# Kernel optimization log

Hardware: AMD Instinct MI355X
Metric: run time of the kernel (lower is better)

Reference implementation:

```python
import jax, jax.numpy as jnp
import numpy as np

NEG = -9.0e15
BN_EPS = 1e-5


def _build_graph():
    N = 22
    A = np.eye(N, dtype=np.float32)
    for i in range(N - 1):
        A[i, i + 1] = 1.0
        A[i + 1, i] = 1.0
    distal = [3, 7, 11, 15, 16, 20, 21]
    jl = [0, 1, 2, 3, 17, 18, 19, 20, 21]
    jr = [4, 5, 6, 7, 12, 13, 14, 15, 16]
    adj_sym = np.zeros((N, N), dtype=np.float32)
    for i in range(N):
        adj_sym[i, i] = 1.0
        if i in jl:
            adj_sym[i, jr[jl.index(i)]] = 1.0
        if i in jr:
            adj_sym[i, jl[jr.index(i)]] = 1.0
    A1 = A.copy()
    for i in distal:
        A1[i] = 0.0
    A2 = np.linalg.matrix_power(A, 2)
    A3 = np.linalg.matrix_power(A, 3)
    for i in range(N):
        if i not in distal:
            A2[i] = 0.0
            A3[i] = 0.0
    adj_con = A1 + A2 + A3
    return adj_sym, adj_con


def setup_inputs() -> dict:
    key = jax.random.key(0)
    B, T, N, C, O = 64, 50, 22, 64, 64
    adj_sym, adj_con = _build_graph()
    rs, cs = np.nonzero(adj_sym > 0)  # row-major, matches torch nonzero order
    rc, cc = np.nonzero(adj_con > 0)
    ks = jax.random.split(key, 11)
    f32 = jnp.float32
    return {
        "x": jax.random.normal(ks[0], (B, T, N, C), f32),
        "W_sym": 0.1 * jax.random.normal(ks[1], (2, C, O), f32),
        "e_sym": 1.0 + 0.1 * jax.random.normal(ks[2], (O, len(rs)), f32),
        "W_con": 0.1 * jax.random.normal(ks[3], (2, C, O), f32),
        "e_con": 1.0 + 0.1 * jax.random.normal(ks[4], (O, len(rc)), f32),
        "W_dis": 0.1 * jax.random.normal(ks[5], (C, O), f32),
        "att": 0.1 * jax.random.normal(ks[6], (N, N), f32),
        "b_dis": 0.1 * jax.random.normal(ks[7], (O,), f32),
        "cat_w": 0.05 * jax.random.normal(ks[8], (O, 3 * O), f32),
        "gammas": 1.0 + 0.1 * jax.random.normal(ks[9], (4, O), f32),
        "betas": 0.1 * jax.random.normal(ks[10], (4, O), f32),
        "rows_sym": jnp.asarray(rs, jnp.int32),
        "cols_sym": jnp.asarray(cs, jnp.int32),
        "rows_con": jnp.asarray(rc, jnp.int32),
        "cols_con": jnp.asarray(cc, jnp.int32),
    }


def _semch(x, W, e, rows, cols):
    # x: [B,T,N,C], W: [2,C,O], e: [O,nnz] -> [B,T,N,O]
    N = x.shape[2]
    O = W.shape[2]
    h0 = x @ W[0]  # [B,T,N,O]
    h1 = x @ W[1]
    logits = jnp.full((O, N, N), NEG, x.dtype).at[:, rows, cols].set(e)
    A = jax.nn.softmax(logits, axis=2)  # per-channel masked softmax over rows
    diag = A[:, jnp.arange(N), jnp.arange(N)]  # [O,N]
    A_off = A * (1.0 - jnp.eye(N, dtype=x.dtype))
    return h0 * diag.T[None, None] + jnp.einsum('cij,btjc->btic', A_off, h1)


def _bn_relu(h, g, b):
    # training-mode BatchNorm2d over [B,C,T,N], stats on (0,2,3)
    mu = h.mean(axis=(0, 2, 3), keepdims=True)
    var = ((h - mu) ** 2).mean(axis=(0, 2, 3), keepdims=True)
    out = (h - mu) * jax.lax.rsqrt(var + BN_EPS) * g[None, :, None, None] + b[None, :, None, None]
    return jax.nn.relu(out)


def reference(x, W_sym, e_sym, W_con, e_con, W_dis, att, b_dis, cat_w,
              gammas, betas, rows_sym, cols_sym, rows_con, cols_con):
    xs = _semch(x, W_sym, e_sym, rows_sym, cols_sym)  # [B,T,N,O]
    yc = _semch(x, W_con, e_con, rows_con, cols_con)  # [B,T,N,O]
    # pairwise distance branch: pos_rel [B,T,N,N,C], summed over dim 2
    pos_rel = x[:, :, :, None, :] - x[:, :, None, :, :]
    dis = jnp.sqrt(jnp.sum(pos_rel * pos_rel, axis=2)) + 1e-8  # [B,T,N,C]
    z = jnp.einsum('ij,btjo->btio', att, dis @ W_dis) + b_dis  # GraphConvolution
    # to NCHW: [B,O,T,N]
    xp = _bn_relu(xs.transpose(0, 3, 1, 2), gammas[0], betas[0])
    yp = _bn_relu(yc.transpose(0, 3, 1, 2), gammas[1], betas[1])
    zp = _bn_relu(z.transpose(0, 3, 1, 2), gammas[2], betas[2])
    cat = jnp.concatenate((xp, yp, zp), axis=1)  # [B,3O,T,N]
    out = jnp.einsum('of,bftn->botn', cat_w, cat)  # 1x1 conv
    out = _bn_relu(out, gammas[3], betas[3])
    return out.transpose(0, 2, 3, 1)  # [B,T,N,O]
```

## Files before the change

kernel.cpp:

```cpp
#include <hip/hip_runtime.h>
#include <hip/hip_bf16.h>

typedef __hip_bfloat16 bf16;
typedef __attribute__((ext_vector_type(8))) short bf16x8;
typedef __attribute__((ext_vector_type(4))) float f32x4;

#define BT     3200
#define N_     22
#define NO     1408
#define NN     484
#define BTN    70400
#define ELEMS  4505600
#define MAXNZ  128
#define NSHARD 16

static __device__ __forceinline__ bf16  f2bf(float v) { return __float2bfloat16(v); }
static __device__ __forceinline__ short fbf(float v) {
    bf16 h = __float2bfloat16(v);
    return *reinterpret_cast<short*>(&h);
}
static __device__ __forceinline__ float sbf(short s) {
    return __uint_as_float(((unsigned)(unsigned short)s) << 16);
}
static __device__ __forceinline__ void unp(unsigned u, float& lo, float& hi) {
    lo = __uint_as_float(u << 16);
    hi = __uint_as_float(u & 0xffff0000u);
}

__global__ void prep_kernel(const float* __restrict__ e_s, const int* __restrict__ rs,
                            const int* __restrict__ cs, int nnz_s,
                            const float* __restrict__ e_c, const int* __restrict__ rc,
                            const int* __restrict__ cc, int nnz_c,
                            const float* __restrict__ cat_w,
                            const float* __restrict__ Wsym, const float* __restrict__ Wcon,
                            const float* __restrict__ Wdis, const float* __restrict__ att,
                            short* __restrict__ AAb, short* __restrict__ CB,
                            short* __restrict__ WB, int* __restrict__ bm,
                            short* __restrict__ attF) {
    const int tid = threadIdx.x;
    if (blockIdx.x < 2) {
        __shared__ float eL[64 * (MAXNZ + 1)];
        __shared__ int rowsL[MAXNZ], colsL[MAXNZ];
        const int t = blockIdx.x;
        const float* e    = t ? e_c : e_s;
        const int*   rows = t ? rc  : rs;
        const int*   cols = t ? cc  : cs;
        const int    nnz  = t ? nnz_c : nnz_s;
        const int    str  = nnz + 1;

        for (int idx = tid; idx < 64 * nnz; idx += 256) {
            int o = idx / nnz, k = idx - o * nnz;
            eL[o * str + k] = expf(e[idx]);
        }
        for (int idx = tid; idx < nnz; idx += 256) { rowsL[idx] = rows[idx]; colsL[idx] = cols[idx]; }
        __syncthreads();

        const int o = tid & 63, ig = tid >> 6;
        float s[6];
        #pragma unroll
        for (int q = 0; q < 6; q++) s[q] = 0.f;
        for (int k = 0; k < nnz; k++) {
            int r = rowsL[k];
            float ev = eL[o * str + k];
            #pragma unroll
            for (int q = 0; q < 6; q++)
                if (r == ig + 4 * q) s[q] += ev;
        }
        float inv[6];
        #pragma unroll
        for (int q = 0; q < 6; q++) inv[q] = 1.f / s[q];
        for (int k = 0; k < nnz; k++) {
            int r = rowsL[k];
            #pragma unroll
            for (int q = 0; q < 6; q++)
                if (r == ig + 4 * q)
                    AAb[((size_t)(r * N_ + colsL[k]) * 64 + o) * 2 + t] =
                        fbf(eL[o * str + k] * inv[q]);
        }
    } else if (blockIdx.x < 8) {
        int gi = (blockIdx.x - 2) * 256 + tid;
        if (gi >= 1536) return;
        int nt = gi / 384, rem = gi % 384;
        int kc = rem >> 6, L = rem & 63;
        int n = nt * 16 + (L & 15);
        int kbase = kc * 32 + (L >> 4) * 8;
        float4 w0 = *(const float4*)&cat_w[n * 192 + kbase];
        float4 w1 = *(const float4*)&cat_w[n * 192 + kbase + 4];
        bf16x8 frag;
        frag[0] = fbf(w0.x); frag[1] = fbf(w0.y); frag[2] = fbf(w0.z); frag[3] = fbf(w0.w);
        frag[4] = fbf(w1.x); frag[5] = fbf(w1.y); frag[6] = fbf(w1.z); frag[7] = fbf(w1.w);
        ((bf16x8*)CB)[gi] = frag;
    } else if (blockIdx.x < 18) {
        int gi = (blockIdx.x - 8) * 256 + tid;
        if (gi >= 2560) return;
        int L = gi & 63;
        int q = gi >> 6;
        int nt = q & 3;
        int pk = q >> 2;
        int kc = pk & 1;
        int p  = pk >> 1;
        const float* Wsrc = (p == 0) ? Wsym :
                            (p == 1) ? Wsym + 4096 :
                            (p == 2) ? Wcon :
                            (p == 3) ? Wcon + 4096 : Wdis;
        int n  = nt * 16 + (L & 15);
        int kb = kc * 32 + (L >> 4) * 8;
        bf16x8 frag;
        #pragma unroll
        for (int j = 0; j < 8; j++) frag[j] = fbf(Wsrc[(kb + j) * 64 + n]);
        ((bf16x8*)WB)[gi] = frag;
    } else {
        if (tid < N_) {
            unsigned bits = 0u;
            for (int e = 0; e < nnz_s; e++)
                if (rs[e] == tid && cs[e] != tid) bits |= 1u << cs[e];
            for (int e = 0; e < nnz_c; e++)
                if (rc[e] == tid && cc[e] != tid) bits |= 1u << cc[e];
            bm[tid] = (int)bits;
        }
        for (int f = tid; f < 128; f += 256) {
            int rt = f >> 6, LL = f & 63;
            int row = rt * 16 + (LL & 15);
            int kb  = (LL >> 4) * 8;
            bf16x8 frag;
            #pragma unroll
            for (int j = 0; j < 8; j++) {
                int k = kb + j;
                float vv = (row < N_ && k < N_) ? att[row * N_ + k] : 0.f;
                frag[j] = fbf(vv);
            }
            ((bf16x8*)attF)[f] = frag;
        }
    }
}

__launch_bounds__(256)
__global__ void fused_hmix(const float* __restrict__ x, const short* __restrict__ WB,
                           const short* __restrict__ AAb, const short* __restrict__ attF,
                           const int* __restrict__ bm, const float* __restrict__ bdis,
                           bf16* __restrict__ xs, bf16* __restrict__ yc,
                           bf16* __restrict__ z, float* __restrict__ stats1) {
    __shared__ __align__(16) char smem[14080];
    short*    xl   = (short*)smem;
    short*    dl   = (short*)(smem + 4096);
    float*    red4 = (float*)(smem + 8192);
    unsigned* pp0  = (unsigned*)smem;
    unsigned* pp1  = (unsigned*)(smem + 5632);
    short*    p2   = (short*)(smem + 11264);
    float*    red  = (float*)smem;

    const int g   = blockIdx.x;
    const int tid = threadIdx.x;
    const size_t base = (size_t)g * NO;
    const int w = tid >> 6, L = tid & 63;
    const int lane16 = L & 15, quad = L >> 4;
    const int colw = w * 16 + lane16;
    const bf16x8* WBf = (const bf16x8*)WB;

    float v[6], s = 0.f, s2 = 0.f;
    #pragma unroll
    for (int k = 0; k < 6; k++) {
        int i = w + 4 * k;
        float t = (i < N_) ? x[base + i * 64 + L] : 0.f;
        v[k] = t; s += t; s2 += t * t;
    }
    red4[w * 64 + L]       = s;
    red4[256 + w * 64 + L] = s2;
    for (int idx = tid; idx < 320; idx += 256) {
        ((unsigned*)xl)[704 + idx] = 0u;
        ((unsigned*)dl)[704 + idx] = 0u;
    }
    __syncthreads();
    float S  = (red4[L] + red4[64 + L]) + (red4[128 + L] + red4[192 + L]);
    float S2 = (red4[256 + L] + red4[320 + L]) + (red4[384 + L] + red4[448 + L]);
    #pragma unroll
    for (int k = 0; k < 6; k++) {
        int i = w + 4 * k;
        if (i < N_) {
            float t = v[k];
            float d2 = S2 - 2.f * t * S + (float)N_ * t * t;
            float d  = sqrtf(fmaxf(d2, 0.f)) + 1e-8f;
            int ci = i * 64 + (L ^ ((i & 7) << 3));
            xl[ci] = fbf(t);
            dl[ci] = fbf(d);
        }
    }
    __syncthreads();

    f32x4 acc[5][2];
    #pragma unroll
    for (int p = 0; p < 5; p++)
        #pragma unroll
        for (int rt = 0; rt < 2; rt++) acc[p][rt] = (f32x4){0.f, 0.f, 0.f, 0.f};

    #pragma unroll
    for (int kc = 0; kc < 2; kc++) {
        bf16x8 ax[2], ad[2];
        #pragma unroll
        for (int rt = 0; rt < 2; rt++) {
            int row = rt * 16 + lane16;
            int ci  = row * 64 + ((kc * 32 + quad * 8) ^ ((row & 7) << 3));
            ax[rt] = *(const bf16x8*)(xl + ci);
            ad[rt] = *(const bf16x8*)(dl + ci);
        }
        #pragma unroll
        for (int p = 0; p < 5; p++) {
            bf16x8 bw = WBf[((p * 2 + kc) * 4 + w) * 64 + L];
            #pragma unroll
            for (int rt = 0; rt < 2; rt++) {
                bf16x8 a = (p < 4) ? ax[rt] : ad[rt];
                acc[p][rt] = __builtin_amdgcn_mfma_f32_16x16x32_bf16(a, bw, acc[p][rt], 0, 0, 0);
            }
        }
    }
    __syncthreads();

    #pragma unroll
    for (int rt = 0; rt < 2; rt++)
        #pragma unroll
        for (int r = 0; r < 4; r++) {
            int m = rt * 16 + quad * 4 + r;
            if (m < N_) {
                float h0s = acc[0][rt][r], h1s = acc[1][rt][r];
                float h0c = acc[2][rt][r], h1c = acc[3][rt][r];
                pp0[m * 64 + colw] = (unsigned)(unsigned short)fbf(h1s) |
                                     ((unsigned)(unsigned short)fbf(h0s) << 16);
                pp1[m * 64 + colw] = (unsigned)(unsigned short)fbf(h1c) |
                                     ((unsigned)(unsigned short)fbf(h0c) << 16);
                p2[m * 64 + colw] = fbf(acc[4][rt][r]);
            }
        }
    __syncthreads();

    f32x4 zacc[2];
    zacc[0] = (f32x4){0.f, 0.f, 0.f, 0.f};
    zacc[1] = (f32x4){0.f, 0.f, 0.f, 0.f};
    {
        bf16x8 bfrag;
        #pragma unroll
        for (int j = 0; j < 8; j++) {
            int k = quad * 8 + j;
            bfrag[j] = (k < N_) ? p2[k * 64 + colw] : (short)0;
        }
        const bf16x8* attFf = (const bf16x8*)attF;
        #pragma unroll
        for (int rt = 0; rt < 2; rt++)
            zacc[rt] = __builtin_amdgcn_mfma_f32_16x16x32_bf16(attFf[rt * 64 + L], bfrag,
                                                               zacc[rt], 0, 0, 0);
    }

    float mxs[6], myc[6];
    #pragma unroll
    for (int k = 0; k < 6; k++) { mxs[k] = 0.f; myc[k] = 0.f; }
    const unsigned* AAu = (const unsigned*)AAb;
    #pragma unroll
    for (int k = 0; k < 6; k++) {
        int i = w + 4 * k;
        if (i < N_) {
            unsigned bits = (unsigned)bm[i];
            while (bits) {
                int j = __ffs(bits) - 1;
                bits &= bits - 1;
                unsigned a = AAu[(size_t)(i * N_ + j) * 64 + L];
                float as, ac; unp(a, as, ac);
                float h1s = sbf((short)pp0[j * 64 + L]);
                float h1c = sbf((short)pp1[j * 64 + L]);
                mxs[k] = fmaf(as, h1s, mxs[k]);
                myc[k] = fmaf(ac, h1c, myc[k]);
            }
        }
    }

    float st0 = 0.f, st1 = 0.f, st2 = 0.f, st3 = 0.f;
    #pragma unroll
    for (int k = 0; k < 6; k++) {
        int i = w + 4 * k;
        if (i < N_) {
            unsigned ad2 = AAu[(size_t)(i * 23) * 64 + L];
            float asd, acd; unp(ad2, asd, acd);
            float h0sv = __uint_as_float(pp0[i * 64 + L] & 0xffff0000u);
            float h0cv = __uint_as_float(pp1[i * 64 + L] & 0xffff0000u);
            float xsv = mxs[k] + asd * h0sv;
            float ycv = myc[k] + acd * h0cv;
            size_t oi = base + i * 64 + L;
            xs[oi] = f2bf(xsv); yc[oi] = f2bf(ycv);
            st0 += xsv; st1 += xsv * xsv;
            st2 += ycv; st3 += ycv * ycv;
        }
    }

    float bd = bdis[colw];
    float st4 = 0.f, st5 = 0.f;
    #pragma unroll
    for (int rt = 0; rt < 2; rt++)
        #pragma unroll
        for (int r = 0; r < 4; r++) {
            int m = rt * 16 + quad * 4 + r;
            if (m < N_) {
                float zv = zacc[rt][r] + bd;
                z[base + (size_t)m * 64 + colw] = f2bf(zv);
                st4 += zv; st5 += zv * zv;
            }
        }
    st4 += __shfl_xor(st4, 16); st4 += __shfl_xor(st4, 32);
    st5 += __shfl_xor(st5, 16); st5 += __shfl_xor(st5, 32);

    __syncthreads();
    red[(w * 4 + 0) * 64 + L] = st0;
    red[(w * 4 + 1) * 64 + L] = st1;
    red[(w * 4 + 2) * 64 + L] = st2;
    red[(w * 4 + 3) * 64 + L] = st3;
    if (quad == 0) { red[16 * 64 + colw] = st4; red[17 * 64 + colw] = st5; }
    __syncthreads();
    float* myStats = stats1 + (size_t)(g & (NSHARD - 1)) * 384;
    for (int qq = tid; qq < 384; qq += 256) {
        int q = qq >> 6, o = qq & 63;
        float vv;
        if (q < 4)
            vv = (red[q * 64 + o] + red[(4 + q) * 64 + o]) +
                 (red[(8 + q) * 64 + o] + red[(12 + q) * 64 + o]);
        else
            vv = red[(12 + q) * 64 + o];
        atomicAdd(&myStats[qq], vv);
    }
}

__global__ void scale_from_stats(const float* __restrict__ stats,
                                 const float* __restrict__ gammas,
                                 const float* __restrict__ betas,
                                 int nch, int gbase, int nshard, int sstride,
                                 float* __restrict__ scale) {
    int tid = threadIdx.x;
    if (tid >= nch * 64) return;
    int t = tid >> 6, o = tid & 63;
    float S = 0.f, SS = 0.f;
    for (int s = 0; s < nshard; s++) {
        S  += stats[s * sstride + (2 * t) * 64 + o];
        SS += stats[s * sstride + (2 * t + 1) * 64 + o];
    }
    const float invn = 1.f / (float)BTN;
    float mu   = S * invn;
    float var  = SS * invn - mu * mu;
    float rstd = rsqrtf(var + 1e-5f);
    float a = gammas[(gbase + t) * 64 + o] * rstd;
    float c = betas[(gbase + t) * 64 + o] - mu * a;
    scale[t * 128 + o]      = a;
    scale[t * 128 + 64 + o] = c;
}

__launch_bounds__(256)
__global__ void mix_pass(const bf16* __restrict__ xs, const bf16* __restrict__ yc,
                         const bf16* __restrict__ z, const float* __restrict__ scale1,
                         const short* __restrict__ CB,
                         bf16* __restrict__ out2, float* __restrict__ stats2) {
    __shared__ float sL[384];
    __shared__ float red[512];

    const int tid = threadIdx.x;
    const int w = tid >> 6, L = tid & 63;
    const int lane16 = L & 15, quad = L >> 4;
    const int R0 = blockIdx.x * 128 + w * 32;

    for (int idx = tid; idx < 384; idx += 256) sL[idx] = scale1[idx];
    __syncthreads();

    const bf16* srcs[3] = { xs, yc, z };

    f32x4 acc[2][4];
    #pragma unroll
    for (int rt = 0; rt < 2; rt++)
        #pragma unroll
        for (int nt = 0; nt < 4; nt++)
            acc[rt][nt] = (f32x4){0.f, 0.f, 0.f, 0.f};

    #pragma unroll
    for (int kc = 0; kc < 6; kc++) {
        const int src = kc >> 1;
        const int c0  = (kc & 1) * 32 + quad * 8;
        bf16x8 av[2];
        #pragma unroll
        for (int rt = 0; rt < 2; rt++) {
            int row = R0 + rt * 16 + lane16;
            uint4 u = *(const uint4*)(srcs[src] + (size_t)row * 64 + c0);
            float v[8];
            unp(u.x, v[0], v[1]); unp(u.y, v[2], v[3]);
            unp(u.z, v[4], v[5]); unp(u.w, v[6], v[7]);
            #pragma unroll
            for (int e = 0; e < 8; e++) {
                float t = fmaxf(fmaf(v[e], sL[src * 128 + c0 + e],
                                     sL[src * 128 + 64 + c0 + e]), 0.f);
                av[rt][e] = fbf(t);
            }
        }
        #pragma unroll
        for (int nt = 0; nt < 4; nt++) {
            bf16x8 bw = ((const bf16x8*)CB)[(nt * 6 + kc) * 64 + L];
            acc[0][nt] = __builtin_amdgcn_mfma_f32_16x16x32_bf16(av[0], bw, acc[0][nt], 0, 0, 0);
            acc[1][nt] = __builtin_amdgcn_mfma_f32_16x16x32_bf16(av[1], bw, acc[1][nt], 0, 0, 0);
        }
    }

    float s[4]  = {0.f, 0.f, 0.f, 0.f};
    float s2[4] = {0.f, 0.f, 0.f, 0.f};
    #pragma unroll
    for (int rt = 0; rt < 2; rt++)
        #pragma unroll
        for (int nt = 0; nt < 4; nt++)
            #pragma unroll
            for (int r = 0; r < 4; r++) {
                int row = R0 + rt * 16 + quad * 4 + r;
                int col = nt * 16 + lane16;
                float v = acc[rt][nt][r];
                out2[(size_t)row * 64 + col] = f2bf(v);
                s[nt] += v; s2[nt] += v * v;
            }
    #pragma unroll
    for (int nt = 0; nt < 4; nt++) {
        s[nt]  += __shfl_xor(s[nt], 16);
        s[nt]  += __shfl_xor(s[nt], 32);
        s2[nt] += __shfl_xor(s2[nt], 16);
        s2[nt] += __shfl_xor(s2[nt], 32);
    }
    if (quad == 0) {
        #pragma unroll
        for (int nt = 0; nt < 4; nt++) {
            red[w * 64 + nt * 16 + lane16]       = s[nt];
            red[256 + w * 64 + nt * 16 + lane16] = s2[nt];
        }
    }
    __syncthreads();
    if (tid < 64) {
        float t = red[tid] + red[64 + tid] + red[128 + tid] + red[192 + tid];
        atomicAdd(&stats2[tid], t);
    } else if (tid < 128) {
        int c = tid - 64;
        float t = red[256 + c] + red[320 + c] + red[384 + c] + red[448 + c];
        atomicAdd(&stats2[64 + c], t);
    }
}

__global__ void final_pass(const bf16* __restrict__ out2, const float* __restrict__ scale2,
                           float* __restrict__ out) {
    const int gid = blockIdx.x * 256 + threadIdx.x;
    const int idx = gid * 4;
    ushort4 u = reinterpret_cast<const ushort4*>(out2)[gid];
    const int o = idx & 63;
    float f0, f1, f2, f3;
    unp((unsigned)u.x | ((unsigned)u.y << 16), f0, f1);
    unp((unsigned)u.z | ((unsigned)u.w << 16), f2, f3);
    float4 r;
    r.x = fmaxf(fmaf(f0, scale2[o],     scale2[64 + o]),     0.f);
    r.y = fmaxf(fmaf(f1, scale2[o + 1], scale2[64 + o + 1]), 0.f);
    r.z = fmaxf(fmaf(f2, scale2[o + 2], scale2[64 + o + 2]), 0.f);
    r.w = fmaxf(fmaf(f3, scale2[o + 3], scale2[64 + o + 3]), 0.f);
    reinterpret_cast<float4*>(out)[gid] = r;
}

extern "C" void kernel_launch(void* const* d_in, const int* in_sizes, int n_in,
                              void* d_out, int out_size, void* d_ws, size_t ws_size,
                              hipStream_t stream) {
    const float* x      = (const float*)d_in[0];
    const float* W_sym  = (const float*)d_in[1];
    const float* e_sym  = (const float*)d_in[2];
    const float* W_con  = (const float*)d_in[3];
    const float* e_con  = (const float*)d_in[4];
    const float* W_dis  = (const float*)d_in[5];
    const float* att    = (const float*)d_in[6];
    const float* b_dis  = (const float*)d_in[7];
    const float* cat_w  = (const float*)d_in[8];
    const float* gammas = (const float*)d_in[9];
    const float* betas  = (const float*)d_in[10];
    const int* rows_sym = (const int*)d_in[11];
    const int* cols_sym = (const int*)d_in[12];
    const int* rows_con = (const int*)d_in[13];
    const int* cols_con = (const int*)d_in[14];
    const int nnz_s = in_sizes[2] / 64;
    const int nnz_c = in_sizes[4] / 64;

    char* p = (char*)d_ws;
    float* stats  = (float*)p; p += (NSHARD * 384 + 128) * 4;
    float* scale1 = (float*)p; p += 384 * 4;
    float* scale2 = (float*)p; p += 128 * 4;
    short* AAb    = (short*)p; p += (size_t)NN * 64 * 2 * 2;
    short* CB     = (short*)p; p += (size_t)1536 * 8 * 2;
    short* WB     = (short*)p; p += (size_t)2560 * 8 * 2;
    int*   bm     = (int*)p;   p += 128;
    short* attF   = (short*)p; p += 128 * 16;
    bf16*  xsb    = (bf16*)p;  p += (size_t)ELEMS * 2;
    bf16*  ycb    = (bf16*)p;  p += (size_t)ELEMS * 2;
    bf16*  zb     = (bf16*)p;  p += (size_t)ELEMS * 2;
    bf16*  out2   = (bf16*)p;  p += (size_t)ELEMS * 2;
    float* stats1 = stats;
    float* stats2 = stats + NSHARD * 384;

    hipMemsetAsync(stats, 0, (NSHARD * 384 + 128) * 4, stream);
    hipMemsetAsync(AAb, 0, (size_t)NN * 64 * 2 * 2, stream);
    prep_kernel<<<19, 256, 0, stream>>>(e_sym, rows_sym, cols_sym, nnz_s,
                                        e_con, rows_con, cols_con, nnz_c,
                                        cat_w, W_sym, W_con, W_dis, att,
                                        AAb, CB, WB, bm, attF);
    fused_hmix<<<BT, 256, 0, stream>>>(x, WB, AAb, attF, bm, b_dis,
                                       xsb, ycb, zb, stats1);
    scale_from_stats<<<1, 192, 0, stream>>>(stats1, gammas, betas, 3, 0, NSHARD, 384, scale1);
    mix_pass<<<550, 256, 0, stream>>>(xsb, ycb, zb, scale1, CB, out2, stats2);
    scale_from_stats<<<1, 64, 0, stream>>>(stats2, gammas, betas, 1, 3, 1, 0, scale2);
    final_pass<<<ELEMS / 1024, 256, 0, stream>>>(out2, scale2, (float*)d_out);
}
```

Baseline: 199.2 us.

## Fold stats scaling into consumers, drop memset, unroll sparse neighbor loop

Removes both scale_from_stats launches and computes the BN scale/shift at the start of every mix_pass and final_pass block, and moves the stats memset into prep_kernel. The variable bitmask while-loop becomes a fixed 8-entry neighbor list padded with a neighbor whose adjacency weight is zero, held in LDS. mix_pass is halved to 16 rows per wave across 1100 blocks, stats2 atomics are sharded eight ways, and final_pass handles four vectors per thread. This trades redundant per-block stats reduction and padded neighbor FMAs for fewer launches and less atomic contention.

```diff
diff --git a/kernel.cpp b/kernel.cpp
--- a/kernel.cpp
+++ b/kernel.cpp
@@ -13,6 +13,7 @@
 #define ELEMS  4505600
 #define MAXNZ  128
 #define NSHARD 16
+#define STATSZ (NSHARD * 384 + 8 * 128)
 
 static __device__ __forceinline__ bf16  f2bf(float v) { return __float2bfloat16(v); }
 static __device__ __forceinline__ short fbf(float v) {
@@ -35,8 +36,8 @@
                             const float* __restrict__ Wsym, const float* __restrict__ Wcon,
                             const float* __restrict__ Wdis, const float* __restrict__ att,
                             short* __restrict__ AAb, short* __restrict__ CB,
-                            short* __restrict__ WB, int* __restrict__ bm,
-                            short* __restrict__ attF) {
+                            short* __restrict__ WB, int* __restrict__ ej,
+                            short* __restrict__ attF, float* __restrict__ stats) {
     const int tid = threadIdx.x;
     if (blockIdx.x < 2) {
         __shared__ float eL[64 * (MAXNZ + 1)];
@@ -110,13 +111,19 @@
         for (int j = 0; j < 8; j++) frag[j] = fbf(Wsrc[(kb + j) * 64 + n]);
         ((bf16x8*)WB)[gi] = frag;
     } else {
+        for (int idx = tid; idx < STATSZ; idx += 256) stats[idx] = 0.f;
         if (tid < N_) {
             unsigned bits = 0u;
             for (int e = 0; e < nnz_s; e++)
                 if (rs[e] == tid && cs[e] != tid) bits |= 1u << cs[e];
             for (int e = 0; e < nnz_c; e++)
                 if (rc[e] == tid && cc[e] != tid) bits |= 1u << cc[e];
-            bm[tid] = (int)bits;
+            int cnt = 0;
+            unsigned b = bits;
+            while (b) { int j = __ffs(b) - 1; b &= b - 1; ej[tid * 8 + cnt++] = j; }
+            int js = 0;
+            while (((bits >> js) & 1u) || js == tid) js++;
+            for (; cnt < 8; cnt++) ej[tid * 8 + cnt] = js;
         }
         for (int f = tid; f < 128; f += 256) {
             int rt = f >> 6, LL = f & 63;
@@ -137,16 +144,17 @@
 __launch_bounds__(256)
 __global__ void fused_hmix(const float* __restrict__ x, const short* __restrict__ WB,
                            const short* __restrict__ AAb, const short* __restrict__ attF,
-                           const int* __restrict__ bm, const float* __restrict__ bdis,
+                           const int* __restrict__ ej, const float* __restrict__ bdis,
                            bf16* __restrict__ xs, bf16* __restrict__ yc,
                            bf16* __restrict__ z, float* __restrict__ stats1) {
-    __shared__ __align__(16) char smem[14080];
+    __shared__ __align__(16) char smem[14784];
     short*    xl   = (short*)smem;
     short*    dl   = (short*)(smem + 4096);
     float*    red4 = (float*)(smem + 8192);
     unsigned* pp0  = (unsigned*)smem;
     unsigned* pp1  = (unsigned*)(smem + 5632);
     short*    p2   = (short*)(smem + 11264);
+    int*      ejL  = (int*)(smem + 14080);
     float*    red  = (float*)smem;
 
     const int g   = blockIdx.x;
@@ -157,6 +165,7 @@
     const int colw = w * 16 + lane16;
     const bf16x8* WBf = (const bf16x8*)WB;
 
+    if (tid < 176) ejL[tid] = ej[tid];
     float v[6], s = 0.f, s2 = 0.f;
     #pragma unroll
     for (int k = 0; k < 6; k++) {
@@ -257,16 +266,13 @@
     for (int k = 0; k < 6; k++) {
         int i = w + 4 * k;
         if (i < N_) {
-            unsigned bits = (unsigned)bm[i];
-            while (bits) {
-                int j = __ffs(bits) - 1;
-                bits &= bits - 1;
+            #pragma unroll
+            for (int e = 0; e < 8; e++) {
+                int j = ejL[i * 8 + e];
                 unsigned a = AAu[(size_t)(i * N_ + j) * 64 + L];
                 float as, ac; unp(a, as, ac);
-                float h1s = sbf((short)pp0[j * 64 + L]);
-                float h1c = sbf((short)pp1[j * 64 + L]);
-                mxs[k] = fmaf(as, h1s, mxs[k]);
-                myc[k] = fmaf(ac, h1c, myc[k]);
+                mxs[k] = fmaf(as, sbf((short)pp0[j * 64 + L]), mxs[k]);
+                myc[k] = fmaf(ac, sbf((short)pp1[j * 64 + L]), myc[k]);
             }
         }
     }
@@ -325,32 +331,10 @@
     }
 }
 
-__global__ void scale_from_stats(const float* __restrict__ stats,
-                                 const float* __restrict__ gammas,
-                                 const float* __restrict__ betas,
-                                 int nch, int gbase, int nshard, int sstride,
-                                 float* __restrict__ scale) {
-    int tid = threadIdx.x;
-    if (tid >= nch * 64) return;
-    int t = tid >> 6, o = tid & 63;
-    float S = 0.f, SS = 0.f;
-    for (int s = 0; s < nshard; s++) {
-        S  += stats[s * sstride + (2 * t) * 64 + o];
-        SS += stats[s * sstride + (2 * t + 1) * 64 + o];
-    }
-    const float invn = 1.f / (float)BTN;
-    float mu   = S * invn;
-    float var  = SS * invn - mu * mu;
-    float rstd = rsqrtf(var + 1e-5f);
-    float a = gammas[(gbase + t) * 64 + o] * rstd;
-    float c = betas[(gbase + t) * 64 + o] - mu * a;
-    scale[t * 128 + o]      = a;
-    scale[t * 128 + 64 + o] = c;
-}
-
 __launch_bounds__(256)
 __global__ void mix_pass(const bf16* __restrict__ xs, const bf16* __restrict__ yc,
-                         const bf16* __restrict__ z, const float* __restrict__ scale1,
+                         const bf16* __restrict__ z, const float* __restrict__ stats1,
+                         const float* __restrict__ gammas, const float* __restrict__ betas,
                          const short* __restrict__ CB,
                          bf16* __restrict__ out2, float* __restrict__ stats2) {
     __shared__ float sL[384];
@@ -359,61 +343,67 @@
     const int tid = threadIdx.x;
     const int w = tid >> 6, L = tid & 63;
     const int lane16 = L & 15, quad = L >> 4;
-    const int R0 = blockIdx.x * 128 + w * 32;
-
-    for (int idx = tid; idx < 384; idx += 256) sL[idx] = scale1[idx];
+    const int R0 = blockIdx.x * 64 + w * 16;
+
+    if (tid < 192) {
+        int t = tid >> 6, o = tid & 63;
+        float S = 0.f, SS = 0.f;
+        for (int s = 0; s < NSHARD; s++) {
+            S  += stats1[s * 384 + (2 * t) * 64 + o];
+            SS += stats1[s * 384 + (2 * t + 1) * 64 + o];
+        }
+        const float invn = 1.f / (float)BTN;
+        float mu   = S * invn;
+        float var  = SS * invn - mu * mu;
+        float rstd = rsqrtf(var + 1e-5f);
+        float a = gammas[t * 64 + o] * rstd;
+        float c = betas[t * 64 + o] - mu * a;
+        sL[t * 128 + o]      = a;
+        sL[t * 128 + 64 + o] = c;
+    }
     __syncthreads();
 
     const bf16* srcs[3] = { xs, yc, z };
 
-    f32x4 acc[2][4];
-    #pragma unroll
-    for (int rt = 0; rt < 2; rt++)
-        #pragma unroll
-        for (int nt = 0; nt < 4; nt++)
-            acc[rt][nt] = (f32x4){0.f, 0.f, 0.f, 0.f};
+    f32x4 acc[4];
+    #pragma unroll
+    for (int nt = 0; nt < 4; nt++) acc[nt] = (f32x4){0.f, 0.f, 0.f, 0.f};
 
     #pragma unroll
     for (int kc = 0; kc < 6; kc++) {
         const int src = kc >> 1;
         const int c0  = (kc & 1) * 32 + quad * 8;
-        bf16x8 av[2];
-        #pragma unroll
-        for (int rt = 0; rt < 2; rt++) {
-            int row = R0 + rt * 16 + lane16;
-            uint4 u = *(const uint4*)(srcs[src] + (size_t)row * 64 + c0);
-            float v[8];
-            unp(u.x, v[0], v[1]); unp(u.y, v[2], v[3]);
-            unp(u.z, v[4], v[5]); unp(u.w, v[6], v[7]);
-            #pragma unroll
-            for (int e = 0; e < 8; e++) {
-                float t = fmaxf(fmaf(v[e], sL[src * 128 + c0 + e],
-                                     sL[src * 128 + 64 + c0 + e]), 0.f);
-                av[rt][e] = fbf(t);
-            }
+        int row = R0 + lane16;
+        uint4 u = *(const uint4*)(srcs[src] + (size_t)row * 64 + c0);
+        float v[8];
+        unp(u.x, v[0], v[1]); unp(u.y, v[2], v[3]);
+        unp(u.z, v[4], v[5]); unp(u.w, v[6], v[7]);
+        bf16x8 av;
+        #pragma unroll
+        for (int e = 0; e < 8; e++) {
+            float t = fmaxf(fmaf(v[e], sL[src * 128 + c0 + e],
+                                 sL[src * 128 + 64 + c0 + e]), 0.f);
+            av[e] = fbf(t);
         }
         #pragma unroll
         for (int nt = 0; nt < 4; nt++) {
             bf16x8 bw = ((const bf16x8*)CB)[(nt * 6 + kc) * 64 + L];
-            acc[0][nt] = __builtin_amdgcn_mfma_f32_16x16x32_bf16(av[0], bw, acc[0][nt], 0, 0, 0);
-            acc[1][nt] = __builtin_amdgcn_mfma_f32_16x16x32_bf16(av[1], bw, acc[1][nt], 0, 0, 0);
+            acc[nt] = __builtin_amdgcn_mfma_f32_16x16x32_bf16(av, bw, acc[nt], 0, 0, 0);
         }
     }
 
     float s[4]  = {0.f, 0.f, 0.f, 0.f};
     float s2[4] = {0.f, 0.f, 0.f, 0.f};
     #pragma unroll
-    for (int rt = 0; rt < 2; rt++)
-        #pragma unroll
-        for (int nt = 0; nt < 4; nt++)
-            #pragma unroll
-            for (int r = 0; r < 4; r++) {
-                int row = R0 + rt * 16 + quad * 4 + r;
-                int col = nt * 16 + lane16;
-                float v = acc[rt][nt][r];
-                out2[(size_t)row * 64 + col] = f2bf(v);
-                s[nt] += v; s2[nt] += v * v;
-            }
+    for (int nt = 0; nt < 4; nt++)
+        #pragma unroll
+        for (int r = 0; r < 4; r++) {
+            int row = R0 + quad * 4 + r;
+            int col = nt * 16 + lane16;
+            float v = acc[nt][r];
+            out2[(size_t)row * 64 + col] = f2bf(v);
+            s[nt] += v; s2[nt] += v * v;
+        }
     #pragma unroll
     for (int nt = 0; nt < 4; nt++) {
         s[nt]  += __shfl_xor(s[nt], 16);
@@ -429,31 +419,55 @@
         }
     }
     __syncthreads();
+    float* myStats = stats2 + (size_t)(blockIdx.x & 7) * 128;
     if (tid < 64) {
         float t = red[tid] + red[64 + tid] + red[128 + tid] + red[192 + tid];
-        atomicAdd(&stats2[tid], t);
+        atomicAdd(&myStats[tid], t);
     } else if (tid < 128) {
         int c = tid - 64;
         float t = red[256 + c] + red[320 + c] + red[384 + c] + red[448 + c];
-        atomicAdd(&stats2[64 + c], t);
-    }
-}
-
-__global__ void final_pass(const bf16* __restrict__ out2, const float* __restrict__ scale2,
+        atomicAdd(&myStats[64 + c], t);
+    }
+}
+
+__launch_bounds__(256)
+__global__ void final_pass(const bf16* __restrict__ out2, const float* __restrict__ stats2,
+                           const float* __restrict__ gammas, const float* __restrict__ betas,
                            float* __restrict__ out) {
-    const int gid = blockIdx.x * 256 + threadIdx.x;
-    const int idx = gid * 4;
-    ushort4 u = reinterpret_cast<const ushort4*>(out2)[gid];
-    const int o = idx & 63;
-    float f0, f1, f2, f3;
-    unp((unsigned)u.x | ((unsigned)u.y << 16), f0, f1);
-    unp((unsigned)u.z | ((unsigned)u.w << 16), f2, f3);
-    float4 r;
-    r.x = fmaxf(fmaf(f0, scale2[o],     scale2[64 + o]),     0.f);
-    r.y = fmaxf(fmaf(f1, scale2[o + 1], scale2[64 + o + 1]), 0.f);
-    r.z = fmaxf(fmaf(f2, scale2[o + 2], scale2[64 + o + 2]), 0.f);
-    r.w = fmaxf(fmaf(f3, scale2[o + 3], scale2[64 + o + 3]), 0.f);
-    reinterpret_cast<float4*>(out)[gid] = r;
+    __shared__ float sc[128];
+    const int tid = threadIdx.x;
+    if (tid < 64) {
+        int o = tid;
+        float S = 0.f, SS = 0.f;
+        for (int s = 0; s < 8; s++) {
+            S  += stats2[s * 128 + o];
+            SS += stats2[s * 128 + 64 + o];
+        }
+        const float invn = 1.f / (float)BTN;
+        float mu   = S * invn;
+        float var  = SS * invn - mu * mu;
+        float rstd = rsqrtf(var + 1e-5f);
+        float a = gammas[192 + o] * rstd;
+        float c = betas[192 + o] - mu * a;
+        sc[o]      = a;
+        sc[64 + o] = c;
+    }
+    __syncthreads();
+    #pragma unroll
+    for (int j = 0; j < 4; j++) {
+        int gid = blockIdx.x * 1024 + j * 256 + tid;
+        ushort4 u = reinterpret_cast<const ushort4*>(out2)[gid];
+        const int o = (gid * 4) & 63;
+        float f0, f1, f2, f3;
+        unp((unsigned)u.x | ((unsigned)u.y << 16), f0, f1);
+        unp((unsigned)u.z | ((unsigned)u.w << 16), f2, f3);
+        float4 r;
+        r.x = fmaxf(fmaf(f0, sc[o],     sc[64 + o]),     0.f);
+        r.y = fmaxf(fmaf(f1, sc[o + 1], sc[64 + o + 1]), 0.f);
+        r.z = fmaxf(fmaf(f2, sc[o + 2], sc[64 + o + 2]), 0.f);
+        r.w = fmaxf(fmaf(f3, sc[o + 3], sc[64 + o + 3]), 0.f);
+        reinterpret_cast<float4*>(out)[gid] = r;
+    }
 }
 
 extern "C" void kernel_launch(void* const* d_in, const int* in_sizes, int n_in,
@@ -478,13 +492,11 @@
     const int nnz_c = in_sizes[4] / 64;
 
     char* p = (char*)d_ws;
-    float* stats  = (float*)p; p += (NSHARD * 384 + 128) * 4;
-    float* scale1 = (float*)p; p += 384 * 4;
-    float* scale2 = (float*)p; p += 128 * 4;
+    float* stats  = (float*)p; p += (size_t)STATSZ * 4;
     short* AAb    = (short*)p; p += (size_t)NN * 64 * 2 * 2;
     short* CB     = (short*)p; p += (size_t)1536 * 8 * 2;
     short* WB     = (short*)p; p += (size_t)2560 * 8 * 2;
-    int*   bm     = (int*)p;   p += 128;
+    int*   ej     = (int*)p;   p += 192 * 4;
     short* attF   = (short*)p; p += 128 * 16;
     bf16*  xsb    = (bf16*)p;  p += (size_t)ELEMS * 2;
     bf16*  ycb    = (bf16*)p;  p += (size_t)ELEMS * 2;
@@ -493,16 +505,14 @@
     float* stats1 = stats;
     float* stats2 = stats + NSHARD * 384;
 
-    hipMemsetAsync(stats, 0, (NSHARD * 384 + 128) * 4, stream);
     hipMemsetAsync(AAb, 0, (size_t)NN * 64 * 2 * 2, stream);
     prep_kernel<<<19, 256, 0, stream>>>(e_sym, rows_sym, cols_sym, nnz_s,
                                         e_con, rows_con, cols_con, nnz_c,
                                         cat_w, W_sym, W_con, W_dis, att,
-                                        AAb, CB, WB, bm, attF);
-    fused_hmix<<<BT, 256, 0, stream>>>(x, WB, AAb, attF, bm, b_dis,
+                                        AAb, CB, WB, ej, attF, stats);
+    fused_hmix<<<BT, 256, 0, stream>>>(x, WB, AAb, attF, ej, b_dis,
                                        xsb, ycb, zb, stats1);
-    scale_from_stats<<<1, 192, 0, stream>>>(stats1, gammas, betas, 3, 0, NSHARD, 384, scale1);
-    mix_pass<<<550, 256, 0, stream>>>(xsb, ycb, zb, scale1, CB, out2, stats2);
-    scale_from_stats<<<1, 64, 0, stream>>>(stats2, gammas, betas, 1, 3, 1, 0, scale2);
-    final_pass<<<ELEMS / 1024, 256, 0, stream>>>(out2, scale2, (float*)d_out);
-}
+    mix_pass<<<1100, 256, 0, stream>>>(xsb, ycb, zb, stats1, gammas, betas,
+                                       CB, out2, stats2);
+    final_pass<<<1100, 256, 0, stream>>>(out2, stats2, gammas, betas, (float*)d_out);
+}
```

New measurement: 172.6 us. 1.15x faster.
